# Optimization experiments

Hardware: AMD Instinct MI355X
Metric: run time of the kernel (lower is better)

The kernel has to match this reference:

```python
import jax, jax.numpy as jnp
import numpy as np

ALPHA = 1.0      # focal_alpha
GAMMA = 2.0      # focal_gamma
MARGIN = 0.3     # triplet_margin
T = 3.0          # kd_temperature
FW, TW, KW = 1.0, 0.5, 1.0  # focal/triplet/kd weights
NEG_INF_FILL = 1000000.0


def setup_inputs() -> dict:
    key = jax.random.key(0)
    k1, k2, k3, k4 = jax.random.split(key, 4)
    B, D, C = 4096, 512, 2
    return {
        "logits": jax.random.normal(k1, (B, C), jnp.float32),
        "features": jax.random.normal(k2, (B, D), jnp.float32),
        "hard_labels": jax.random.randint(k3, (B,), 0, 2),
        "soft_labels": jax.random.uniform(k4, (B, C), jnp.float32),
    }


def _pairwise_dist(x):
    # torch.cdist(x, x, p=2): [B, B] euclidean distances, safe sqrt (grad-safe at 0)
    sq = jnp.sum(x * x, axis=1)
    d2 = jnp.maximum(sq[:, None] + sq[None, :] - 2.0 * (x @ x.T), 0.0)
    safe = jnp.where(d2 > 0, d2, 1.0)
    return jnp.where(d2 > 0, jnp.sqrt(safe), 0.0)


def reference(logits, features, hard_labels, soft_labels):
    B = logits.shape[0]
    # ---- focal loss (integer-label branch) ----
    logp = jax.nn.log_softmax(logits, axis=-1)
    ce = -jnp.take_along_axis(logp, hard_labels[:, None], axis=1)[:, 0]
    pt = jnp.exp(-ce)
    focal = jnp.mean(ALPHA * (1.0 - pt) ** GAMMA * ce)

    # ---- triplet loss: batch-hard mining, vectorized over rows ----
    d = _pairwise_dist(features)                      # [B, B]
    same = hard_labels[:, None] == hard_labels[None, :]
    eye = jnp.eye(B, dtype=bool)
    mpos = (same & ~eye).astype(d.dtype)              # positives, diag zeroed
    mneg = (~same).astype(d.dtype)                    # negatives
    posd = d * mpos
    valid = (jnp.sum(posd, axis=1) > 0).astype(d.dtype)
    hardest_pos = jnp.max(posd, axis=1)
    hardest_neg = jnp.min(d * mneg + (1.0 - mneg) * NEG_INF_FILL, axis=1)
    per_row = jax.nn.relu(hardest_pos - hardest_neg + MARGIN)
    n_valid = jnp.sum(valid)
    triplet = jnp.where(n_valid > 0,
                        jnp.sum(per_row * valid) / jnp.maximum(n_valid, 1.0),
                        0.0)

    # ---- KD loss: KLDiv(batchmean) * T^2 ----
    student_log = jax.nn.log_softmax(logits / T, axis=-1)
    teacher = jax.nn.softmax(jnp.log(soft_labels + 1e-8) / T, axis=-1)
    kd = jnp.sum(teacher * (jnp.log(teacher) - student_log)) / B * (T ** 2)

    total = FW * focal + TW * triplet + KW * kd
    return total, focal, triplet, kd
```

## Files before the change

### kernel.cpp

```cpp
#include <hip/hip_runtime.h>
#include <hip/hip_bf16.h>

#define B_ROWS 4096
#define D_FEAT 512

typedef short s16x8 __attribute__((ext_vector_type(8)));
typedef float f32x4 __attribute__((ext_vector_type(4)));

#define GLOAD_LDS16(gsrc, ldst)                                                        \
    __builtin_amdgcn_global_load_lds(                                                  \
        (const __attribute__((address_space(1))) void*)(gsrc),                         \
        (__attribute__((address_space(3))) void*)(ldst), 16, 0, 0)

__device__ inline float waveReduceSum(float v) {
#pragma unroll
    for (int off = 32; off > 0; off >>= 1) v += __shfl_xor(v, off);
    return v;
}

__global__ __launch_bounds__(256) void prep_kernel(const float* __restrict__ feat,
                                                   const float* __restrict__ logits,
                                                   const int* __restrict__ labels,
                                                   const float* __restrict__ soft,
                                                   short* __restrict__ featbf,
                                                   float* __restrict__ sqn,
                                                   unsigned* __restrict__ posmax,
                                                   float* __restrict__ negminf,
                                                   float* __restrict__ fpart,
                                                   float* __restrict__ kpart) {
    const int bid = blockIdx.x, tid = threadIdx.x;
    const int wave = tid >> 6, lane = tid & 63;
    const int row = bid * 4 + wave;

    const float* p = feat + (size_t)row * D_FEAT + lane * 8;
    float4 a = *(const float4*)p;
    float4 b = *(const float4*)(p + 4);
    float vals[8] = {a.x, a.y, a.z, a.w, b.x, b.y, b.z, b.w};
    short outv[8];
    float s = 0.f;
#pragma unroll
    for (int j = 0; j < 8; ++j) {
        __hip_bfloat16 h = __float2bfloat16(vals[j]);
        outv[j] = *(short*)&h;
        float xb = __bfloat162float(h);
        s = fmaf(xb, xb, s);
    }
    *(s16x8*)(featbf + (size_t)row * D_FEAT + lane * 8) = *(s16x8*)outv;
    s = waveReduceSum(s);
    if (lane == 0) sqn[row] = s;

    if (tid < 4) posmax[bid * 4 + tid] = 0u;
    else if (tid < 8) negminf[bid * 4 + tid - 4] = 1e12f;

    if (bid < 16) {
        int i = bid * 256 + tid;
        float l0 = logits[2 * i], l1 = logits[2 * i + 1];

        float m = fmaxf(l0, l1);
        float lse = m + logf(expf(l0 - m) + expf(l1 - m));
        float lp = (labels[i] ? l1 : l0) - lse;
        float ce = -lp;
        float pt = expf(lp);
        float om = 1.f - pt;
        float focal = om * om * ce;

        const float Tinv = 1.f / 3.f;
        float s0 = l0 * Tinv, s1 = l1 * Tinv;
        float ms = fmaxf(s0, s1);
        float lses = ms + logf(expf(s0 - ms) + expf(s1 - ms));
        float sl0 = s0 - lses, sl1 = s1 - lses;
        float t0 = logf(soft[2 * i] + 1e-8f) * Tinv;
        float t1 = logf(soft[2 * i + 1] + 1e-8f) * Tinv;
        float mt = fmaxf(t0, t1);
        float lset = mt + logf(expf(t0 - mt) + expf(t1 - mt));
        float tl0 = t0 - lset, tl1 = t1 - lset;
        float p0 = expf(tl0), p1 = expf(tl1);
        float kd = p0 * (tl0 - sl0) + p1 * (tl1 - sl1);

        float fs = waveReduceSum(focal);
        float ks = waveReduceSum(kd);
        __shared__ float sf[4], sk[4];
        if (lane == 0) { sf[wave] = fs; sk[wave] = ks; }
        __syncthreads();
        if (tid == 0) {
            fpart[bid] = sf[0] + sf[1] + sf[2] + sf[3];
            kpart[bid] = sk[0] + sk[1] + sk[2] + sk[3];
        }
    }
}

__global__ __launch_bounds__(512) void pairwise_8ph_kernel(const short* __restrict__ featbf,
                                                           const float* __restrict__ sqn,
                                                           const int* __restrict__ labels,
                                                           unsigned* __restrict__ posmax,
                                                           unsigned* __restrict__ negmin) {
    __shared__ short As0[256 * 64], As1[256 * 64];
    __shared__ short Bs0[256 * 64], Bs1[256 * 64];
    const int tid = threadIdx.x;
    const int bfl = blockIdx.x;
    const int xcd = bfl & 7, loc = bfl >> 3;
    const int ib = (xcd & 3) * 4 + (loc & 3);
    const int jb = ((xcd >> 1) & 2) * 4 + (loc >> 2);
    const int wid = tid >> 6, lane = tid & 63;
    const int wr = wid >> 2, wc = wid & 3;
    const int lo = lane & 15, hi = lane >> 4;

    const int rbA0 = (wid < 4) ? wid * 16 : 64 + wid * 16;
    const int rbB0 = wid * 16;
    const int rA0 = rbA0 + (lane >> 2), rA1 = rA0 + 64;
    const int rB0 = rbB0 + (lane >> 2), rB1 = rB0 + 128;
    const int cA0 = (lane & 3) ^ ((rA0 >> 1) & 3), cA1 = (lane & 3) ^ ((rA1 >> 1) & 3);
    const int cB0 = (lane & 3) ^ ((rB0 >> 1) & 3), cB1 = (lane & 3) ^ ((rB1 >> 1) & 3);
    const short* gA0 = featbf + (size_t)(ib * 256 + rA0) * D_FEAT + cA0 * 8;
    const short* gA1 = featbf + (size_t)(ib * 256 + rA1) * D_FEAT + cA1 * 8;
    const short* gB0 = featbf + (size_t)(jb * 256 + rB0) * D_FEAT + cB0 * 8;
    const short* gB1 = featbf + (size_t)(jb * 256 + rB1) * D_FEAT + cB1 * 8;
    const int dA0 = rbA0 * 32, dA1 = (rbA0 + 64) * 32;
    const int dB0 = rbB0 * 32, dB1 = (rbB0 + 128) * 32;

#define ISSUE(gptr, buf, dstbase, ksv, ktv)                                            \
    GLOAD_LDS16((gptr) + (ktv) * 64 + (ksv) * 32, (buf) + (ksv) * 8192 + (dstbase))

    int aoffs[8], boffs[4];
#pragma unroll
    for (int m = 0; m < 8; ++m) {
        int r = wr * 128 + m * 16 + lo;
        aoffs[m] = r * 32 + ((hi ^ ((r >> 1) & 3)) * 8);
    }
#pragma unroll
    for (int n = 0; n < 4; ++n) {
        int r = wc * 64 + n * 16 + lo;
        boffs[n] = r * 32 + ((hi ^ ((r >> 1) & 3)) * 8);
    }

    f32x4 acc[8][4];
#pragma unroll
    for (int m = 0; m < 8; ++m)
#pragma unroll
        for (int n = 0; n < 4; ++n)
            acc[m][n] = (f32x4){0.f, 0.f, 0.f, 0.f};

#define PHASE(mh, ksv, DO_BFR, ISSUES, VMCNT)                                          \
    {                                                                                  \
        if (DO_BFR) {                                                                  \
            _Pragma("unroll") for (int n = 0; n < 4; ++n)                              \
                bfr[n] = *(const s16x8*)(Bcur + (ksv) * 8192 + boffs[n]);              \
        }                                                                              \
        s16x8 af[4];                                                                   \
        _Pragma("unroll") for (int mi = 0; mi < 4; ++mi)                               \
            af[mi] = *(const s16x8*)(Acur + (ksv) * 8192 + aoffs[(mh) * 4 + mi]);      \
        ISSUES;                                                                        \
        __builtin_amdgcn_s_barrier();                                                  \
        __builtin_amdgcn_sched_barrier(0);                                             \
        __builtin_amdgcn_s_setprio(1);                                                 \
        _Pragma("unroll") for (int mi = 0; mi < 4; ++mi)                               \
            _Pragma("unroll") for (int n = 0; n < 4; ++n)                              \
                acc[(mh) * 4 + mi][n] = __builtin_amdgcn_mfma_f32_16x16x32_bf16(       \
                    af[mi], bfr[n], acc[(mh) * 4 + mi][n], 0, 0, 0);                   \
        __builtin_amdgcn_s_setprio(0);                                                 \
        VMCNT;                                                                         \
        __builtin_amdgcn_s_barrier();                                                  \
        __builtin_amdgcn_sched_barrier(0);                                             \
    }

#define VM(n) asm volatile("s_waitcnt vmcnt(" #n ")" ::: "memory")

    const short* Acur = As0;
    const short* Bcur = Bs0;
    short* Anxt = As1;
    short* Bnxt = Bs1;

    ISSUE(gA0, As0, dA0, 0, 0);
    ISSUE(gB0, Bs0, dB0, 0, 0);
    ISSUE(gB1, Bs0, dB1, 0, 0);
    ISSUE(gA1, As0, dA1, 0, 0);
    ISSUE(gA0, As0, dA0, 1, 0);
    ISSUE(gB0, Bs0, dB0, 1, 0);
    ISSUE(gB1, Bs0, dB1, 1, 0);
    ISSUE(gA1, As0, dA1, 1, 0);
    VM(5);
    __builtin_amdgcn_s_barrier();
    __builtin_amdgcn_sched_barrier(0);

#pragma unroll 1
    for (int kt = 0; kt < D_FEAT / 64 - 1; ++kt) {
        s16x8 bfr[4];
        PHASE(0, 0, true,
              { ISSUE(gA0, Anxt, dA0, 0, kt + 1); ISSUE(gB0, Bnxt, dB0, 0, kt + 1); },
              VM(6));
        PHASE(1, 0, false,
              { ISSUE(gB1, Bnxt, dB1, 0, kt + 1); ISSUE(gA1, Anxt, dA1, 0, kt + 1); },
              VM(5));
        PHASE(0, 1, true,
              { ISSUE(gA0, Anxt, dA0, 1, kt + 1); ISSUE(gB0, Bnxt, dB0, 1, kt + 1); },
              VM(6));
        PHASE(1, 1, false,
              { ISSUE(gB1, Bnxt, dB1, 1, kt + 1); ISSUE(gA1, Anxt, dA1, 1, kt + 1); },
              VM(5));
        const short* t1 = Acur; Acur = Anxt; Anxt = (short*)t1;
        const short* t2 = Bcur; Bcur = Bnxt; Bnxt = (short*)t2;
    }
    {
        s16x8 bfr[4];
        PHASE(0, 0, true,  {}, VM(4));
        PHASE(1, 0, false, {}, VM(1));
        PHASE(0, 1, true,  {}, VM(0));
        PHASE(1, 1, false, {}, {});
    }

#undef PHASE
#undef VM
#undef ISSUE

    int coln[4], labc[4];
    float sqc[4];
#pragma unroll
    for (int n = 0; n < 4; ++n) {
        coln[n] = jb * 256 + wc * 64 + n * 16 + lo;
        labc[n] = labels[coln[n]];
        sqc[n] = sqn[coln[n]];
    }
    __syncthreads();
    float (*redp)[5] = (float(*)[5])As0;
    float (*redn)[5] = ((float(*)[5])As0) + 256;

#pragma unroll
    for (int m = 0; m < 8; ++m) {
#pragma unroll
        for (int r = 0; r < 4; ++r) {
            int row_loc = wr * 128 + m * 16 + hi * 4 + r;
            int row_g = ib * 256 + row_loc;
            int labr = labels[row_g];
            float sqr = sqn[row_g];
            float pm = 0.f, nm = 1e12f;
#pragma unroll
            for (int n = 0; n < 4; ++n) {
                float d2 = fmaxf(sqr + fmaf(-2.f, acc[m][n][r], sqc[n]), 0.f);
                bool same = (labr == labc[n]);
                if (same) {
                    if (row_g != coln[n]) pm = fmaxf(pm, d2);
                } else {
                    nm = fminf(nm, d2);
                }
            }
#pragma unroll
            for (int off = 1; off < 16; off <<= 1) {
                pm = fmaxf(pm, __shfl_xor(pm, off));
                nm = fminf(nm, __shfl_xor(nm, off));
            }
            if (lo == 0) {
                redp[row_loc][wc] = pm;
                redn[row_loc][wc] = nm;
            }
        }
    }
    __syncthreads();
    if (tid < 256) {
        float p = fmaxf(fmaxf(redp[tid][0], redp[tid][1]),
                        fmaxf(redp[tid][2], redp[tid][3]));
        atomicMax(&posmax[ib * 256 + tid], __float_as_uint(p));
    } else {
        int row = tid - 256;
        float nn = fminf(fminf(redn[row][0], redn[row][1]),
                         fminf(redn[row][2], redn[row][3]));
        atomicMin(&negmin[ib * 256 + row], __float_as_uint(nn));
    }
}

__global__ __launch_bounds__(256) void finalize_kernel(const unsigned* __restrict__ posmax,
                                                       const unsigned* __restrict__ negmin,
                                                       const float* __restrict__ fpart,
                                                       const float* __restrict__ kpart,
                                                       float* __restrict__ out) {
    int tid = threadIdx.x;
    float sum_pr = 0.f, sum_v = 0.f;
    for (int i = tid; i < B_ROWS; i += 256) {
        float p2 = __uint_as_float(posmax[i]);
        float n2 = __uint_as_float(negmin[i]);
        float v = (p2 > 0.f) ? 1.f : 0.f;
        sum_pr += fmaxf(sqrtf(p2) - sqrtf(n2) + 0.3f, 0.f) * v;
        sum_v += v;
    }
    sum_pr = waveReduceSum(sum_pr);
    sum_v = waveReduceSum(sum_v);
    __shared__ float sp[4], sv[4];
    int wave = tid >> 6, lane = tid & 63;
    if (lane == 0) { sp[wave] = sum_pr; sv[wave] = sum_v; }
    __syncthreads();
    if (tid == 0) {
        float spr = sp[0] + sp[1] + sp[2] + sp[3];
        float svv = sv[0] + sv[1] + sv[2] + sv[3];
        float fsum = 0.f, ksum = 0.f;
        for (int b = 0; b < 16; ++b) { fsum += fpart[b]; ksum += kpart[b]; }
        float focal = fsum / 4096.f;
        float kd = ksum / 4096.f * 9.f;
        float triplet = (svv > 0.f) ? spr / fmaxf(svv, 1.f) : 0.f;
        float total = focal + 0.5f * triplet + kd;
        out[0] = total;
        out[1] = focal;
        out[2] = triplet;
        out[3] = kd;
    }
}

extern "C" void kernel_launch(void* const* d_in, const int* in_sizes, int n_in,
                              void* d_out, int out_size, void* d_ws, size_t ws_size,
                              hipStream_t stream) {
    const float* logits = (const float*)d_in[0];
    const float* feat   = (const float*)d_in[1];
    const int*   labels = (const int*)d_in[2];
    const float* soft   = (const float*)d_in[3];

    char* ws = (char*)d_ws;
    unsigned* posmax = (unsigned*)ws;
    unsigned* negmin = (unsigned*)(ws + 16384);
    float*    sqn    = (float*)(ws + 32768);
    float*    fpart  = (float*)(ws + 49152);
    float*    kpart  = (float*)(ws + 49152 + 256);
    short*    featbf = (short*)(ws + 65536);

    prep_kernel<<<1024, 256, 0, stream>>>(feat, logits, labels, soft, featbf, sqn,
                                          posmax, (float*)negmin, fpart, kpart);
    pairwise_8ph_kernel<<<256, 512, 0, stream>>>(featbf, sqn, labels, posmax, negmin);
    finalize_kernel<<<1, 256, 0, stream>>>(posmax, negmin, fpart, kpart,
                                           (float*)d_out);
}
```

Measured before the change: 44.23 us.

## Use 16 waves per block for pairwise GEMM with smaller per-wave tiles

The pairwise distance kernel now launches 1024 threads (16 waves) per 256x256 tile instead of 512 (8 waves). Each wave computes a 64x64 sub-tile instead of 128x64, which halves the accumulator registers and simplifies the load schedule to one A and one B async load per half-k step. The aim is more latency hiding from extra waves per CU. In exchange, each wave does less MFMA work between barriers, the barrier cost grows with more waves, and B fragments are read from LDS twice as often relative to compute.

```diff
diff --git a/kernel.cpp b/kernel.cpp
--- a/kernel.cpp
+++ b/kernel.cpp
@@ -89,11 +89,11 @@
     }
 }
 
-__global__ __launch_bounds__(512) void pairwise_8ph_kernel(const short* __restrict__ featbf,
-                                                           const float* __restrict__ sqn,
-                                                           const int* __restrict__ labels,
-                                                           unsigned* __restrict__ posmax,
-                                                           unsigned* __restrict__ negmin) {
+__global__ __launch_bounds__(1024) void pairwise_16w_kernel(const short* __restrict__ featbf,
+                                                            const float* __restrict__ sqn,
+                                                            const int* __restrict__ labels,
+                                                            unsigned* __restrict__ posmax,
+                                                            unsigned* __restrict__ negmin) {
     __shared__ short As0[256 * 64], As1[256 * 64];
     __shared__ short Bs0[256 * 64], Bs1[256 * 64];
     const int tid = threadIdx.x;
@@ -105,26 +105,19 @@
     const int wr = wid >> 2, wc = wid & 3;
     const int lo = lane & 15, hi = lane >> 4;
 
-    const int rbA0 = (wid < 4) ? wid * 16 : 64 + wid * 16;
-    const int rbB0 = wid * 16;
-    const int rA0 = rbA0 + (lane >> 2), rA1 = rA0 + 64;
-    const int rB0 = rbB0 + (lane >> 2), rB1 = rB0 + 128;
-    const int cA0 = (lane & 3) ^ ((rA0 >> 1) & 3), cA1 = (lane & 3) ^ ((rA1 >> 1) & 3);
-    const int cB0 = (lane & 3) ^ ((rB0 >> 1) & 3), cB1 = (lane & 3) ^ ((rB1 >> 1) & 3);
-    const short* gA0 = featbf + (size_t)(ib * 256 + rA0) * D_FEAT + cA0 * 8;
-    const short* gA1 = featbf + (size_t)(ib * 256 + rA1) * D_FEAT + cA1 * 8;
-    const short* gB0 = featbf + (size_t)(jb * 256 + rB0) * D_FEAT + cB0 * 8;
-    const short* gB1 = featbf + (size_t)(jb * 256 + rB1) * D_FEAT + cB1 * 8;
-    const int dA0 = rbA0 * 32, dA1 = (rbA0 + 64) * 32;
-    const int dB0 = rbB0 * 32, dB1 = (rbB0 + 128) * 32;
-
-#define ISSUE(gptr, buf, dstbase, ksv, ktv)                                            \
-    GLOAD_LDS16((gptr) + (ktv) * 64 + (ksv) * 32, (buf) + (ksv) * 8192 + (dstbase))
-
-    int aoffs[8], boffs[4];
-#pragma unroll
-    for (int m = 0; m < 8; ++m) {
-        int r = wr * 128 + m * 16 + lo;
+    const int srow = wid * 16 + (lane >> 2);
+    const int sc = (lane & 3) ^ ((srow >> 1) & 3);
+    const short* gA = featbf + (size_t)(ib * 256 + srow) * D_FEAT + sc * 8;
+    const short* gB = featbf + (size_t)(jb * 256 + srow) * D_FEAT + sc * 8;
+    const int dst = wid * 512;
+
+#define ISSUE(gptr, buf, ksv, ktv)                                                     \
+    GLOAD_LDS16((gptr) + (ktv) * 64 + (ksv) * 32, (buf) + (ksv) * 8192 + dst)
+
+    int aoffs[4], boffs[4];
+#pragma unroll
+    for (int m = 0; m < 4; ++m) {
+        int r = wr * 64 + m * 16 + lo;
         aoffs[m] = r * 32 + ((hi ^ ((r >> 1) & 3)) * 8);
     }
 #pragma unroll
@@ -133,30 +126,28 @@
         boffs[n] = r * 32 + ((hi ^ ((r >> 1) & 3)) * 8);
     }
 
-    f32x4 acc[8][4];
-#pragma unroll
-    for (int m = 0; m < 8; ++m)
+    f32x4 acc[4][4];
+#pragma unroll
+    for (int m = 0; m < 4; ++m)
 #pragma unroll
         for (int n = 0; n < 4; ++n)
             acc[m][n] = (f32x4){0.f, 0.f, 0.f, 0.f};
 
-#define PHASE(mh, ksv, DO_BFR, ISSUES, VMCNT)                                          \
+#define PHASE(ksv, ISSUES, VMCNT)                                                      \
     {                                                                                  \
-        if (DO_BFR) {                                                                  \
-            _Pragma("unroll") for (int n = 0; n < 4; ++n)                              \
-                bfr[n] = *(const s16x8*)(Bcur + (ksv) * 8192 + boffs[n]);              \
-        }                                                                              \
-        s16x8 af[4];                                                                   \
-        _Pragma("unroll") for (int mi = 0; mi < 4; ++mi)                               \
-            af[mi] = *(const s16x8*)(Acur + (ksv) * 8192 + aoffs[(mh) * 4 + mi]);      \
+        s16x8 af[4], bfr[4];                                                           \
+        _Pragma("unroll") for (int n = 0; n < 4; ++n)                                  \
+            bfr[n] = *(const s16x8*)(Bcur + (ksv) * 8192 + boffs[n]);                  \
+        _Pragma("unroll") for (int m = 0; m < 4; ++m)                                  \
+            af[m] = *(const s16x8*)(Acur + (ksv) * 8192 + aoffs[m]);                   \
         ISSUES;                                                                        \
         __builtin_amdgcn_s_barrier();                                                  \
         __builtin_amdgcn_sched_barrier(0);                                             \
         __builtin_amdgcn_s_setprio(1);                                                 \
-        _Pragma("unroll") for (int mi = 0; mi < 4; ++mi)                               \
+        _Pragma("unroll") for (int m = 0; m < 4; ++m)                                  \
             _Pragma("unroll") for (int n = 0; n < 4; ++n)                              \
-                acc[(mh) * 4 + mi][n] = __builtin_amdgcn_mfma_f32_16x16x32_bf16(       \
-                    af[mi], bfr[n], acc[(mh) * 4 + mi][n], 0, 0, 0);                   \
+                acc[m][n] = __builtin_amdgcn_mfma_f32_16x16x32_bf16(                   \
+                    af[m], bfr[n], acc[m][n], 0, 0, 0);                                \
         __builtin_amdgcn_s_setprio(0);                                                 \
         VMCNT;                                                                         \
         __builtin_amdgcn_s_barrier();                                                  \
@@ -170,42 +161,24 @@
     short* Anxt = As1;
     short* Bnxt = Bs1;
 
-    ISSUE(gA0, As0, dA0, 0, 0);
-    ISSUE(gB0, Bs0, dB0, 0, 0);
-    ISSUE(gB1, Bs0, dB1, 0, 0);
-    ISSUE(gA1, As0, dA1, 0, 0);
-    ISSUE(gA0, As0, dA0, 1, 0);
-    ISSUE(gB0, Bs0, dB0, 1, 0);
-    ISSUE(gB1, Bs0, dB1, 1, 0);
-    ISSUE(gA1, As0, dA1, 1, 0);
-    VM(5);
+    ISSUE(gA, As0, 0, 0);
+    ISSUE(gB, Bs0, 0, 0);
+    ISSUE(gA, As0, 1, 0);
+    ISSUE(gB, Bs0, 1, 0);
+    VM(2);
     __builtin_amdgcn_s_barrier();
     __builtin_amdgcn_sched_barrier(0);
 
 #pragma unroll 1
     for (int kt = 0; kt < D_FEAT / 64 - 1; ++kt) {
-        s16x8 bfr[4];
-        PHASE(0, 0, true,
-              { ISSUE(gA0, Anxt, dA0, 0, kt + 1); ISSUE(gB0, Bnxt, dB0, 0, kt + 1); },
-              VM(6));
-        PHASE(1, 0, false,
-              { ISSUE(gB1, Bnxt, dB1, 0, kt + 1); ISSUE(gA1, Anxt, dA1, 0, kt + 1); },
-              VM(5));
-        PHASE(0, 1, true,
-              { ISSUE(gA0, Anxt, dA0, 1, kt + 1); ISSUE(gB0, Bnxt, dB0, 1, kt + 1); },
-              VM(6));
-        PHASE(1, 1, false,
-              { ISSUE(gB1, Bnxt, dB1, 1, kt + 1); ISSUE(gA1, Anxt, dA1, 1, kt + 1); },
-              VM(5));
+        PHASE(0, { ISSUE(gA, Anxt, 0, kt + 1); ISSUE(gB, Bnxt, 0, kt + 1); }, VM(2));
+        PHASE(1, { ISSUE(gA, Anxt, 1, kt + 1); ISSUE(gB, Bnxt, 1, kt + 1); }, VM(2));
         const short* t1 = Acur; Acur = Anxt; Anxt = (short*)t1;
         const short* t2 = Bcur; Bcur = Bnxt; Bnxt = (short*)t2;
     }
     {
-        s16x8 bfr[4];
-        PHASE(0, 0, true,  {}, VM(4));
-        PHASE(1, 0, false, {}, VM(1));
-        PHASE(0, 1, true,  {}, VM(0));
-        PHASE(1, 1, false, {}, {});
+        PHASE(0, {}, VM(0));
+        PHASE(1, {}, {});
     }
 
 #undef PHASE
@@ -225,10 +198,10 @@
     float (*redn)[5] = ((float(*)[5])As0) + 256;
 
 #pragma unroll
-    for (int m = 0; m < 8; ++m) {
+    for (int m = 0; m < 4; ++m) {
 #pragma unroll
         for (int r = 0; r < 4; ++r) {
-            int row_loc = wr * 128 + m * 16 + hi * 4 + r;
+            int row_loc = wr * 64 + m * 16 + hi * 4 + r;
             int row_g = ib * 256 + row_loc;
             int labr = labels[row_g];
             float sqr = sqn[row_g];
@@ -259,7 +232,7 @@
         float p = fmaxf(fmaxf(redp[tid][0], redp[tid][1]),
                         fmaxf(redp[tid][2], redp[tid][3]));
         atomicMax(&posmax[ib * 256 + tid], __float_as_uint(p));
-    } else {
+    } else if (tid < 512) {
         int row = tid - 256;
         float nn = fminf(fminf(redn[row][0], redn[row][1]),
                          fminf(redn[row][2], redn[row][3]));
@@ -321,7 +294,7 @@
 
     prep_kernel<<<1024, 256, 0, stream>>>(feat, logits, labels, soft, featbf, sqn,
                                           posmax, (float*)negmin, fpart, kpart);
-    pairwise_8ph_kernel<<<256, 512, 0, stream>>>(featbf, sqn, labels, posmax, negmin);
+    pairwise_16w_kernel<<<256, 1024, 0, stream>>>(featbf, sqn, labels, posmax, negmin);
     finalize_kernel<<<1, 256, 0, stream>>>(posmax, negmin, fpart, kpart,
                                            (float*)d_out);
 }
```

Result: faster. 41.91 us (-5.2%).
